# Optimization experiments

Hardware: AMD Instinct MI355X
Metric: run time of the kernel (lower is better)

Reference implementation:

```python
import jax, jax.numpy as jnp
import numpy as np

EPS = 1e-5
N, DEG, D, L = 50000, 16, 128, 2  # nodes, max_neighbor, embed_size, gnn_layer


def _log_map_zero(y):
    # Poincare ball log map at origin: atanh(||y||) * y / ||y||, with clamps
    n = jnp.linalg.norm(y, axis=-1, keepdims=True)
    nc = jnp.clip(n, EPS, 1.0 - EPS)
    return y * (jnp.arctanh(nc) / nc)


def _exp_map_zero(v):
    # Poincare ball exp map at origin: tanh(||v||) * v / ||v||
    n = jnp.linalg.norm(v, axis=-1, keepdims=True)
    nc = jnp.maximum(n, EPS)
    return v * (jnp.tanh(nc) / nc)


def setup_inputs() -> dict:
    key = jax.random.key(0)
    k1, k2, k3, k4, k5 = jax.random.split(key, 5)
    node_repr = jax.random.normal(k1, (N, D), jnp.float32) * 0.1
    adj = jax.random.randint(k2, (N, DEG), 0, N)
    weight = jax.random.normal(k3, (N, DEG), jnp.float32)
    mask = jnp.ones((N, 1), jnp.float32)
    # per-relation, per-layer message weights (2 relations: pos / neg edges)
    scale = 1.0 / np.sqrt(D)
    W_pos = jax.random.normal(k4, (L, D, D), jnp.float32) * scale
    W_neg = jax.random.normal(k5, (L, D, D), jnp.float32) * scale
    return {"node_repr": node_repr, "adj": adj, "weight": weight,
            "mask": mask, "W_pos": W_pos, "W_neg": W_neg}


def reference(node_repr, adj, weight, mask, W_pos, W_neg):
    # split_graph_by_negative_edge
    pos_m = (weight > 0).astype(weight.dtype)
    neg_m = (weight < 0).astype(weight.dtype)
    adjs = (adj * pos_m.astype(adj.dtype), adj * neg_m.astype(adj.dtype))
    ws = (weight * pos_m, (-weight) * neg_m)
    Ws = (W_pos, W_neg)

    x = node_repr
    for step in range(L):
        x = (_log_map_zero(x) if step > 0 else x) * mask
        combined = jnp.zeros_like(x)
        for a, w, W in zip(adjs, ws, Ws):
            msg = (x @ W[step]) * mask                    # [N, D]
            nb = msg[a.reshape(-1)].reshape(N, DEG, D)    # neighbor gather
            combined = combined + jnp.sum(w[..., None] * nb, axis=1)
        combined = combined * mask                        # dropout identity (eval)
        x = _exp_map_zero(combined) * mask
        x = jax.nn.relu(x) * mask                         # poincare activation
    return x
```

## Files before the change

kernel.cpp:

```cpp
#include <hip/hip_runtime.h>
#include <math.h>

#define DD 128
#define DEG 16
#define TM 32
#define LDST 136
#define EPSV 1e-5f

typedef _Float16 half4_t __attribute__((ext_vector_type(4)));
typedef _Float16 half8_t __attribute__((ext_vector_type(8)));
typedef float    f32x4   __attribute__((ext_vector_type(4)));

__global__ void prep_x(const float* __restrict__ x, _Float16* __restrict__ x16, int n4)
{
    int i = blockIdx.x * blockDim.x + threadIdx.x;
    if (i >= n4) return;
    float4 v = ((const float4*)x)[i];
    half4_t h;
    h[0] = (_Float16)v.x; h[1] = (_Float16)v.y; h[2] = (_Float16)v.z; h[3] = (_Float16)v.w;
    ((half4_t*)x16)[i] = h;
}

__global__ void prep_w(const float* __restrict__ Wp, const float* __restrict__ Wn,
                       _Float16* __restrict__ WT)
{
    const int l = blockIdx.x >> 1, rel = blockIdx.x & 1;
    const float* __restrict__ src = (rel ? Wn : Wp) + (size_t)l * DD * DD;
    _Float16* __restrict__ dst = WT + (size_t)blockIdx.x * DD * DD;
    for (int o = threadIdx.x; o < DD * DD; o += blockDim.x) {
        int nn = o >> 7, kk = o & 127;
        dst[o] = (_Float16)src[kk * DD + nn];
    }
}

__global__ __launch_bounds__(128, 4) void fused_layer(
    const _Float16* __restrict__ src16,
    const int*   __restrict__ adj, const float* __restrict__ wgt,
    const float* __restrict__ mask,
    const _Float16* __restrict__ WTp, const _Float16* __restrict__ WTn,
    float* __restrict__ dst_f32, _Float16* __restrict__ dst_f16,
    int n, int apply_logmap)
{
    __shared__ __align__(16) _Float16 aggP[TM][LDST];
    __shared__ __align__(16) _Float16 aggN[TM][LDST];

    const int row0   = blockIdx.x * TM;
    const int tid    = threadIdx.x;
    const int lane32 = tid & 31;
    const int hw     = tid >> 5;

    #pragma unroll
    for (int i = 0; i < 8; ++i) {
        const int r    = hw * 8 + i;
        const int node = row0 + r;
        f32x4 aP = {0.f, 0.f, 0.f, 0.f};
        f32x4 aN = {0.f, 0.f, 0.f, 0.f};
        if (node < n) {
            const int*   __restrict__ arow = adj + (size_t)node * DEG;
            const float* __restrict__ wrow = wgt + (size_t)node * DEG;
            #pragma unroll
            for (int j = 0; j < DEG; ++j) {
                float w   = wrow[j];
                int   idx = arow[j];
                float m   = mask[idx];
                float m2  = m * m;
                float wp  = fmaxf(w, 0.f)  * m2;
                float wn  = fmaxf(-w, 0.f) * m2;
                half4_t v = *(const half4_t*)(src16 + (size_t)idx * DD + lane32 * 4);
                float v0 = (float)v[0], v1 = (float)v[1], v2 = (float)v[2], v3 = (float)v[3];
                aP[0] += wp * v0; aP[1] += wp * v1; aP[2] += wp * v2; aP[3] += wp * v3;
                aN[0] += wn * v0; aN[1] += wn * v1; aN[2] += wn * v2; aN[3] += wn * v3;
            }
        }
        half4_t hP, hN;
        hP[0] = (_Float16)aP[0]; hP[1] = (_Float16)aP[1];
        hP[2] = (_Float16)aP[2]; hP[3] = (_Float16)aP[3];
        hN[0] = (_Float16)aN[0]; hN[1] = (_Float16)aN[1];
        hN[2] = (_Float16)aN[2]; hN[3] = (_Float16)aN[3];
        *(half4_t*)&aggP[r][lane32 * 4] = hP;
        *(half4_t*)&aggN[r][lane32 * 4] = hN;
    }
    __syncthreads();

    const int wv   = tid >> 6;
    const int l64  = tid & 63;
    const int l15  = l64 & 15;
    const int quad = l64 >> 4;

    half8_t aPf[4], aNf[4];
    #pragma unroll
    for (int kb = 0; kb < 4; ++kb) {
        aPf[kb] = *(const half8_t*)&aggP[16 * wv + l15][kb * 32 + quad * 8];
        aNf[kb] = *(const half8_t*)&aggN[16 * wv + l15][kb * 32 + quad * 8];
    }

    f32x4 acc[8];
    #pragma unroll
    for (int nb = 0; nb < 8; ++nb) acc[nb] = (f32x4){0.f, 0.f, 0.f, 0.f};

    #pragma unroll
    for (int nb = 0; nb < 8; ++nb) {
        const _Float16* bp = WTp + (size_t)(nb * 16 + l15) * DD + quad * 8;
        const _Float16* bn = WTn + (size_t)(nb * 16 + l15) * DD + quad * 8;
        #pragma unroll
        for (int kb = 0; kb < 4; ++kb) {
            half8_t bP = *(const half8_t*)(bp + kb * 32);
            half8_t bN = *(const half8_t*)(bn + kb * 32);
            acc[nb] = __builtin_amdgcn_mfma_f32_16x16x32_f16(aPf[kb], bP, acc[nb], 0, 0, 0);
            acc[nb] = __builtin_amdgcn_mfma_f32_16x16x32_f16(aNf[kb], bN, acc[nb], 0, 0, 0);
        }
    }

    #pragma unroll
    for (int r = 0; r < 4; ++r) {
        const int row = row0 + 16 * wv + quad * 4 + r;
        const float m = (row < n) ? mask[row] : 0.f;

        float cv[8];
        float c2 = 0.f;
        #pragma unroll
        for (int nb = 0; nb < 8; ++nb) { cv[nb] = acc[nb][r] * m; c2 += cv[nb] * cv[nb]; }
        c2 += __shfl_xor(c2, 1);
        c2 += __shfl_xor(c2, 2);
        c2 += __shfl_xor(c2, 4);
        c2 += __shfl_xor(c2, 8);
        float nc = fmaxf(sqrtf(c2), EPSV);
        float sc = tanhf(nc) / nc;

        float xv[8];
        float s2 = 0.f;
        #pragma unroll
        for (int nb = 0; nb < 8; ++nb) {
            float t = fmaxf(cv[nb] * sc * m, 0.f) * m;
            xv[nb] = t; s2 += t * t;
        }

        if (apply_logmap) {
            s2 += __shfl_xor(s2, 1);
            s2 += __shfl_xor(s2, 2);
            s2 += __shfl_xor(s2, 4);
            s2 += __shfl_xor(s2, 8);
            float nc2 = fminf(fmaxf(sqrtf(s2), EPSV), 1.f - EPSV);
            float sc2 = atanhf(nc2) / nc2;
            if (row < n) {
                _Float16* drow = dst_f16 + (size_t)row * DD + l15;
                #pragma unroll
                for (int nb = 0; nb < 8; ++nb) drow[nb * 16] = (_Float16)(xv[nb] * sc2);
            }
        } else {
            if (row < n) {
                float* drow = dst_f32 + (size_t)row * DD + l15;
                #pragma unroll
                for (int nb = 0; nb < 8; ++nb) drow[nb * 16] = xv[nb];
            }
        }
    }
}

extern "C" void kernel_launch(void* const* d_in, const int* in_sizes, int n_in,
                              void* d_out, int out_size, void* d_ws, size_t ws_size,
                              hipStream_t stream)
{
    const float* node_repr = (const float*)d_in[0];
    const int*   adj       = (const int*)  d_in[1];
    const float* weight    = (const float*)d_in[2];
    const float* mask      = (const float*)d_in[3];
    const float* W_pos     = (const float*)d_in[4];
    const float* W_neg     = (const float*)d_in[5];

    const int n = in_sizes[0] / DD;

    _Float16* x16 = (_Float16*)d_ws;
    _Float16* y16 = x16 + (size_t)n * DD;
    _Float16* WT  = y16 + (size_t)n * DD;

    const int n4 = n * DD / 4;
    prep_x<<<(n4 + 255) / 256, 256, 0, stream>>>(node_repr, x16, n4);
    prep_w<<<4, 256, 0, stream>>>(W_pos, W_neg, WT);

    dim3 grid((n + TM - 1) / TM);
    fused_layer<<<grid, 128, 0, stream>>>(x16, adj, weight, mask,
                                          WT + 0 * DD * DD, WT + 1 * DD * DD,
                                          nullptr, y16, n, 1);
    fused_layer<<<grid, 128, 0, stream>>>(y16, adj, weight, mask,
                                          WT + 2 * DD * DD, WT + 3 * DD * DD,
                                          (float*)d_out, nullptr, n, 0);
}
```

Before: 210.5 us.

## Shrink row tile, split output columns across waves, batch neighbor gathers

Halves the rows per block to 16 and doubles the block to 256 threads. Each of the four waves now computes two of the eight output column tiles, and the row norms are combined through shared-memory partial sums with extra barriers. The neighbor gather loads indices and weights as vectors and issues eight row loads before accumulating, to raise memory-level parallelism. The neighbor mask factor is folded into the prepared features (prep_x and the layer-1 output) rather than loaded per edge. This gives more blocks and waves to hide gather latency, at the cost of more barriers and a higher per-block share of weight-matrix loads.

```diff
diff --git a/kernel.cpp b/kernel.cpp
--- a/kernel.cpp
+++ b/kernel.cpp
@@ -3,7 +3,7 @@
 
 #define DD 128
 #define DEG 16
-#define TM 32
+#define TM 16
 #define LDST 136
 #define EPSV 1e-5f
 
@@ -11,13 +11,17 @@
 typedef _Float16 half8_t __attribute__((ext_vector_type(8)));
 typedef float    f32x4   __attribute__((ext_vector_type(4)));
 
-__global__ void prep_x(const float* __restrict__ x, _Float16* __restrict__ x16, int n4)
+__global__ void prep_x(const float* __restrict__ x, const float* __restrict__ mask,
+                       _Float16* __restrict__ x16, int n4)
 {
     int i = blockIdx.x * blockDim.x + threadIdx.x;
     if (i >= n4) return;
+    float m = mask[i >> 5];
+    float m2 = m * m;
     float4 v = ((const float4*)x)[i];
     half4_t h;
-    h[0] = (_Float16)v.x; h[1] = (_Float16)v.y; h[2] = (_Float16)v.z; h[3] = (_Float16)v.w;
+    h[0] = (_Float16)(v.x * m2); h[1] = (_Float16)(v.y * m2);
+    h[2] = (_Float16)(v.z * m2); h[3] = (_Float16)(v.w * m2);
     ((half4_t*)x16)[i] = h;
 }
 
@@ -33,7 +37,7 @@
     }
 }
 
-__global__ __launch_bounds__(128, 4) void fused_layer(
+__global__ __launch_bounds__(256, 6) void fused_layer(
     const _Float16* __restrict__ src16,
     const int*   __restrict__ adj, const float* __restrict__ wgt,
     const float* __restrict__ mask,
@@ -43,15 +47,17 @@
 {
     __shared__ __align__(16) _Float16 aggP[TM][LDST];
     __shared__ __align__(16) _Float16 aggN[TM][LDST];
+    __shared__ float partA[4][TM];
+    __shared__ float partB[4][TM];
 
     const int row0   = blockIdx.x * TM;
     const int tid    = threadIdx.x;
     const int lane32 = tid & 31;
-    const int hw     = tid >> 5;
-
-    #pragma unroll
-    for (int i = 0; i < 8; ++i) {
-        const int r    = hw * 8 + i;
+    const int hw2    = tid >> 5;
+
+    #pragma unroll
+    for (int i = 0; i < 2; ++i) {
+        const int r    = hw2 * 2 + i;
         const int node = row0 + r;
         f32x4 aP = {0.f, 0.f, 0.f, 0.f};
         f32x4 aN = {0.f, 0.f, 0.f, 0.f};
@@ -59,17 +65,26 @@
             const int*   __restrict__ arow = adj + (size_t)node * DEG;
             const float* __restrict__ wrow = wgt + (size_t)node * DEG;
             #pragma unroll
-            for (int j = 0; j < DEG; ++j) {
-                float w   = wrow[j];
-                int   idx = arow[j];
-                float m   = mask[idx];
-                float m2  = m * m;
-                float wp  = fmaxf(w, 0.f)  * m2;
-                float wn  = fmaxf(-w, 0.f) * m2;
-                half4_t v = *(const half4_t*)(src16 + (size_t)idx * DD + lane32 * 4);
-                float v0 = (float)v[0], v1 = (float)v[1], v2 = (float)v[2], v3 = (float)v[3];
-                aP[0] += wp * v0; aP[1] += wp * v1; aP[2] += wp * v2; aP[3] += wp * v3;
-                aN[0] += wn * v0; aN[1] += wn * v1; aN[2] += wn * v2; aN[3] += wn * v3;
+            for (int b = 0; b < 2; ++b) {
+                int4   i0 = ((const int4*)arow)[b * 2 + 0];
+                int4   i1 = ((const int4*)arow)[b * 2 + 1];
+                float4 w0 = ((const float4*)wrow)[b * 2 + 0];
+                float4 w1 = ((const float4*)wrow)[b * 2 + 1];
+                const int   idxs[8] = {i0.x, i0.y, i0.z, i0.w, i1.x, i1.y, i1.z, i1.w};
+                const float ws[8]   = {w0.x, w0.y, w0.z, w0.w, w1.x, w1.y, w1.z, w1.w};
+                half4_t v[8];
+                #pragma unroll
+                for (int j = 0; j < 8; ++j)
+                    v[j] = *(const half4_t*)(src16 + (size_t)idxs[j] * DD + lane32 * 4);
+                #pragma unroll
+                for (int j = 0; j < 8; ++j) {
+                    float wp = fmaxf(ws[j], 0.f);
+                    float wn = fmaxf(-ws[j], 0.f);
+                    float v0 = (float)v[j][0], v1 = (float)v[j][1];
+                    float v2 = (float)v[j][2], v3 = (float)v[j][3];
+                    aP[0] += wp * v0; aP[1] += wp * v1; aP[2] += wp * v2; aP[3] += wp * v3;
+                    aN[0] += wn * v0; aN[1] += wn * v1; aN[2] += wn * v2; aN[3] += wn * v3;
+                }
             }
         }
         half4_t hP, hN;
@@ -82,7 +97,7 @@
     }
     __syncthreads();
 
-    const int wv   = tid >> 6;
+    const int wv2  = tid >> 6;
     const int l64  = tid & 63;
     const int l15  = l64 & 15;
     const int quad = l64 >> 4;
@@ -90,69 +105,85 @@
     half8_t aPf[4], aNf[4];
     #pragma unroll
     for (int kb = 0; kb < 4; ++kb) {
-        aPf[kb] = *(const half8_t*)&aggP[16 * wv + l15][kb * 32 + quad * 8];
-        aNf[kb] = *(const half8_t*)&aggN[16 * wv + l15][kb * 32 + quad * 8];
-    }
-
-    f32x4 acc[8];
-    #pragma unroll
-    for (int nb = 0; nb < 8; ++nb) acc[nb] = (f32x4){0.f, 0.f, 0.f, 0.f};
-
-    #pragma unroll
-    for (int nb = 0; nb < 8; ++nb) {
+        aPf[kb] = *(const half8_t*)&aggP[l15][kb * 32 + quad * 8];
+        aNf[kb] = *(const half8_t*)&aggN[l15][kb * 32 + quad * 8];
+    }
+
+    f32x4 acc[2];
+    acc[0] = (f32x4){0.f, 0.f, 0.f, 0.f};
+    acc[1] = (f32x4){0.f, 0.f, 0.f, 0.f};
+    #pragma unroll
+    for (int t = 0; t < 2; ++t) {
+        const int nb = wv2 * 2 + t;
         const _Float16* bp = WTp + (size_t)(nb * 16 + l15) * DD + quad * 8;
         const _Float16* bn = WTn + (size_t)(nb * 16 + l15) * DD + quad * 8;
         #pragma unroll
         for (int kb = 0; kb < 4; ++kb) {
-            half8_t bP = *(const half8_t*)(bp + kb * 32);
-            half8_t bN = *(const half8_t*)(bn + kb * 32);
-            acc[nb] = __builtin_amdgcn_mfma_f32_16x16x32_f16(aPf[kb], bP, acc[nb], 0, 0, 0);
-            acc[nb] = __builtin_amdgcn_mfma_f32_16x16x32_f16(aNf[kb], bN, acc[nb], 0, 0, 0);
-        }
-    }
-
+            acc[t] = __builtin_amdgcn_mfma_f32_16x16x32_f16(
+                aPf[kb], *(const half8_t*)(bp + kb * 32), acc[t], 0, 0, 0);
+            acc[t] = __builtin_amdgcn_mfma_f32_16x16x32_f16(
+                aNf[kb], *(const half8_t*)(bn + kb * 32), acc[t], 0, 0, 0);
+        }
+    }
+
+    float cv0[4], cv1[4], mr[4];
     #pragma unroll
     for (int r = 0; r < 4; ++r) {
-        const int row = row0 + 16 * wv + quad * 4 + r;
-        const float m = (row < n) ? mask[row] : 0.f;
-
-        float cv[8];
-        float c2 = 0.f;
-        #pragma unroll
-        for (int nb = 0; nb < 8; ++nb) { cv[nb] = acc[nb][r] * m; c2 += cv[nb] * cv[nb]; }
-        c2 += __shfl_xor(c2, 1);
-        c2 += __shfl_xor(c2, 2);
-        c2 += __shfl_xor(c2, 4);
-        c2 += __shfl_xor(c2, 8);
+        const int rl  = quad * 4 + r;
+        const int row = row0 + rl;
+        float m = (row < n) ? mask[row] : 0.f;
+        mr[r] = m;
+        float c0 = acc[0][r] * m, c1 = acc[1][r] * m;
+        cv0[r] = c0; cv1[r] = c1;
+        float p = c0 * c0 + c1 * c1;
+        p += __shfl_xor(p, 1); p += __shfl_xor(p, 2);
+        p += __shfl_xor(p, 4); p += __shfl_xor(p, 8);
+        if (l15 == 0) partA[wv2][rl] = p;
+    }
+    __syncthreads();
+
+    float x0[4], x1[4];
+    #pragma unroll
+    for (int r = 0; r < 4; ++r) {
+        const int rl = quad * 4 + r;
+        float c2 = partA[0][rl] + partA[1][rl] + partA[2][rl] + partA[3][rl];
         float nc = fmaxf(sqrtf(c2), EPSV);
         float sc = tanhf(nc) / nc;
-
-        float xv[8];
-        float s2 = 0.f;
+        float m  = mr[r];
+        float t0 = fmaxf(cv0[r] * sc * m, 0.f) * m;
+        float t1 = fmaxf(cv1[r] * sc * m, 0.f) * m;
+        x0[r] = t0; x1[r] = t1;
+        if (apply_logmap) {
+            float p = t0 * t0 + t1 * t1;
+            p += __shfl_xor(p, 1); p += __shfl_xor(p, 2);
+            p += __shfl_xor(p, 4); p += __shfl_xor(p, 8);
+            if (l15 == 0) partB[wv2][rl] = p;
+        }
+    }
+
+    if (apply_logmap) {
+        __syncthreads();
         #pragma unroll
-        for (int nb = 0; nb < 8; ++nb) {
-            float t = fmaxf(cv[nb] * sc * m, 0.f) * m;
-            xv[nb] = t; s2 += t * t;
-        }
-
-        if (apply_logmap) {
-            s2 += __shfl_xor(s2, 1);
-            s2 += __shfl_xor(s2, 2);
-            s2 += __shfl_xor(s2, 4);
-            s2 += __shfl_xor(s2, 8);
+        for (int r = 0; r < 4; ++r) {
+            const int rl  = quad * 4 + r;
+            const int row = row0 + rl;
+            if (row >= n) continue;
+            float s2  = partB[0][rl] + partB[1][rl] + partB[2][rl] + partB[3][rl];
             float nc2 = fminf(fmaxf(sqrtf(s2), EPSV), 1.f - EPSV);
-            float sc2 = atanhf(nc2) / nc2;
-            if (row < n) {
-                _Float16* drow = dst_f16 + (size_t)row * DD + l15;
-                #pragma unroll
-                for (int nb = 0; nb < 8; ++nb) drow[nb * 16] = (_Float16)(xv[nb] * sc2);
-            }
-        } else {
-            if (row < n) {
-                float* drow = dst_f32 + (size_t)row * DD + l15;
-                #pragma unroll
-                for (int nb = 0; nb < 8; ++nb) drow[nb * 16] = xv[nb];
-            }
+            float f = (atanhf(nc2) / nc2) * mr[r] * mr[r];
+            _Float16* drow = dst_f16 + (size_t)row * DD + wv2 * 32 + l15;
+            drow[0]  = (_Float16)(x0[r] * f);
+            drow[16] = (_Float16)(x1[r] * f);
+        }
+    } else {
+        #pragma unroll
+        for (int r = 0; r < 4; ++r) {
+            const int rl  = quad * 4 + r;
+            const int row = row0 + rl;
+            if (row >= n) continue;
+            float* drow = dst_f32 + (size_t)row * DD + wv2 * 32 + l15;
+            drow[0]  = x0[r];
+            drow[16] = x1[r];
         }
     }
 }
@@ -175,14 +206,14 @@
     _Float16* WT  = y16 + (size_t)n * DD;
 
     const int n4 = n * DD / 4;
-    prep_x<<<(n4 + 255) / 256, 256, 0, stream>>>(node_repr, x16, n4);
+    prep_x<<<(n4 + 255) / 256, 256, 0, stream>>>(node_repr, mask, x16, n4);
     prep_w<<<4, 256, 0, stream>>>(W_pos, W_neg, WT);
 
     dim3 grid((n + TM - 1) / TM);
-    fused_layer<<<grid, 128, 0, stream>>>(x16, adj, weight, mask,
+    fused_layer<<<grid, 256, 0, stream>>>(x16, adj, weight, mask,
                                           WT + 0 * DD * DD, WT + 1 * DD * DD,
                                           nullptr, y16, n, 1);
-    fused_layer<<<grid, 128, 0, stream>>>(y16, adj, weight, mask,
+    fused_layer<<<grid, 256, 0, stream>>>(y16, adj, weight, mask,
                                           WT + 2 * DD * DD, WT + 3 * DD * DD,
                                           (float*)d_out, nullptr, n, 0);
 }
```

Result: faster. 204.7 us (-2.8%).
